# Performance work log

Hardware: AMD Instinct MI355X
Metric: run time of the kernel (lower is better)

## Reference

```python
import jax, jax.numpy as jnp
import numpy as np

B, T, C = 2, 2048, 1024
NH, NKV, HD = 16, 4, 64
VEC = 32  # ve_gate_channels


def _rope(x, cos, sin):
    d = x.shape[-1] // 2
    x1, x2 = x[..., :d], x[..., d:]
    return jnp.concatenate([x1 * cos + x2 * sin, -x1 * sin + x2 * cos], axis=-1)


def _rmsnorm(x):
    eps = jnp.finfo(x.dtype).eps
    return x * jax.lax.rsqrt(jnp.mean(x * x, axis=-1, keepdims=True) + eps)


def setup_inputs() -> dict:
    key = jax.random.key(0)
    ks = jax.random.split(key, 9)
    s = 0.02
    return {
        "x": jax.random.normal(ks[0], (B, T, C), jnp.float32),
        "ve": jax.random.normal(ks[1], (B, T, NKV * HD), jnp.float32),
        "cos": jax.random.normal(ks[2], (1, T, 1, HD // 2), jnp.float32),
        "sin": jax.random.normal(ks[3], (1, T, 1, HD // 2), jnp.float32),
        "Wq": jax.random.normal(ks[4], (C, NH * HD), jnp.float32) * s,
        "Wk": jax.random.normal(ks[5], (C, NKV * HD), jnp.float32) * s,
        "Wv": jax.random.normal(ks[6], (C, NKV * HD), jnp.float32) * s,
        "Wproj": jax.random.normal(ks[7], (C, C), jnp.float32) * s,
        "Wgate": jax.random.normal(ks[8], (VEC, NKV), jnp.float32) * s,
        "window_size": 1024,
    }


def reference(x, ve, cos, sin, Wq, Wk, Wv, Wproj, Wgate, window_size):
    Bx, Tx, Cx = x.shape
    q = (x @ Wq).reshape(Bx, Tx, NH, HD)
    k = (x @ Wk).reshape(Bx, Tx, NKV, HD)
    v = (x @ Wv).reshape(Bx, Tx, NKV, HD)

    # value-embedding gate (has_ve True for this layer)
    gate = 2.0 * jax.nn.sigmoid(x[..., :VEC] @ Wgate)  # [B,T,NKV]
    v = v + gate[..., None] * ve.reshape(Bx, Tx, NKV, HD)

    q, k = _rope(q, cos, sin), _rope(k, cos, sin)
    q, k = _rmsnorm(q), _rmsnorm(k)

    q = q.transpose(0, 2, 1, 3)  # [B,NH,T,HD]
    k = k.transpose(0, 2, 1, 3)  # [B,NKV,T,HD]
    v = v.transpose(0, 2, 1, 3)

    # GQA: each KV head serves NH//NKV consecutive q heads
    g = NH // NKV
    k = jnp.repeat(k, g, axis=1)
    v = jnp.repeat(v, g, axis=1)

    row = jnp.arange(Tx)[:, None]
    col = jnp.arange(Tx)[None, :]
    mask = (col <= row) & (col >= row - window_size)  # causal sliding window

    scores = jnp.einsum("bhqd,bhkd->bhqk", q, k) / np.sqrt(HD).astype(np.float32)
    scores = jnp.where(mask[None, None], scores, jnp.finfo(scores.dtype).min)
    attn = jax.nn.softmax(scores, axis=-1)
    y = jnp.einsum("bhqk,bhkd->bhqd", attn, v)

    y = y.transpose(0, 2, 1, 3).reshape(Bx, Tx, Cx)
    return y @ Wproj
```

## Files before the change

kernel.cpp:

```cpp
#include <hip/hip_runtime.h>

typedef __bf16 bf16x8 __attribute__((ext_vector_type(8)));
typedef __bf16 bf16x4 __attribute__((ext_vector_type(4)));
typedef float f32x4 __attribute__((ext_vector_type(4)));

__device__ inline float tof(float v) { return v; }
__device__ inline float tof(__bf16 v) { return (float)v; }

__device__ inline bf16x8 load8(const __bf16* p) { return *(const bf16x8*)p; }
__device__ inline bf16x8 load8(const float* p) {
    const float4 a = *(const float4*)p;
    const float4 b = *(const float4*)(p + 4);
    bf16x8 r;
    r[0] = (__bf16)a.x; r[1] = (__bf16)a.y; r[2] = (__bf16)a.z; r[3] = (__bf16)a.w;
    r[4] = (__bf16)b.x; r[5] = (__bf16)b.y; r[6] = (__bf16)b.z; r[7] = (__bf16)b.w;
    return r;
}

__device__ __forceinline__ float ldT(const void* p, size_t i, int isf32) {
    return isf32 ? ((const float*)p)[i] : tof(((const __bf16*)p)[i]);
}

__device__ __forceinline__ void cp16(__bf16* lds, const __bf16* g) {
    __builtin_amdgcn_global_load_lds((__attribute__((address_space(1))) void*)g,
                                     (__attribute__((address_space(3))) void*)lds,
                                     16, 0, 0);
}

__device__ __forceinline__ int sniff_block(const void* xraw) {
    const unsigned short* xs = (const unsigned short*)xraw;
    int tid = threadIdx.x;
    int bad = 0;
#pragma unroll
    for (int k = 0; k < 2; ++k) {
        float v = __uint_as_float(((unsigned int)xs[tid * 2 + k]) << 16);
        float a = fabsf(v);
        if (!(a <= 1e4f) || (a != 0.f && a < 1e-6f)) bad = 1;
    }
    return __syncthreads_count(bad) > 32;
}

template <typename T>
__device__ __forceinline__ void prep_body(
    const T* __restrict__ Wq, const T* __restrict__ Wk,
    const T* __restrict__ Wv, const T* __restrict__ Wp, const T* __restrict__ Wg,
    __bf16* __restrict__ WqT, __bf16* __restrict__ WkT,
    __bf16* __restrict__ WvT, __bf16* __restrict__ WpT,
    __bf16* __restrict__ wgb, __bf16* tile)
{
    const int b = blockIdx.x, tid = threadIdx.x;
    if (b < 640) {
        int idx = b;
        const T* src; __bf16* dst; int C;
        if (idx < 256)      { src = Wq; dst = WqT; C = 1024; }
        else if (idx < 320) { src = Wk; dst = WkT; C = 256;  idx -= 256; }
        else if (idx < 384) { src = Wv; dst = WvT; C = 256;  idx -= 320; }
        else                { src = Wp; dst = WpT; C = 1024; idx -= 384; }
        const int ctiles = C >> 6;
        const int r0 = (idx / ctiles) * 64, c0 = (idx % ctiles) * 64;
#pragma unroll
        for (int i = 0; i < 2; ++i) {
            int c = tid + i * 256, ir = c >> 3, ic = (c & 7) * 8;
            *(bf16x8*)(&tile[ir * 72 + ic]) = load8(src + (size_t)(r0 + ir) * C + c0 + ic);
        }
        __syncthreads();
#pragma unroll
        for (int i = 0; i < 2; ++i) {
            int c = tid + i * 256, orr = c >> 3, okc = (c & 7) * 8;
            bf16x8 v;
#pragma unroll
            for (int j = 0; j < 8; ++j) v[j] = tile[(okc + j) * 72 + orr];
            *(bf16x8*)(dst + (size_t)(c0 + orr) * 1024 + r0 + okc) = v;
        }
    } else if (tid < 128) {
        wgb[tid] = (__bf16)tof(Wg[tid]);
    }
}

__global__ __launch_bounds__(256) void prep_kernel(
    const void* x,
    const void* Wq, const void* Wk, const void* Wv, const void* Wp, const void* Wg,
    __bf16* WqT, __bf16* WkT, __bf16* WvT, __bf16* WpT, __bf16* wgb)
{
    __shared__ __bf16 tile[64 * 72];
    const int isf32 = sniff_block(x);
    if (isf32) {
        prep_body<float>((const float*)Wq, (const float*)Wk, (const float*)Wv,
                         (const float*)Wp, (const float*)Wg,
                         WqT, WkT, WvT, WpT, wgb, tile);
    } else {
        prep_body<__bf16>((const __bf16*)Wq, (const __bf16*)Wk, (const __bf16*)Wv,
                          (const __bf16*)Wp, (const __bf16*)Wg,
                          WqT, WkT, WvT, WpT, wgb, tile);
    }
}

__global__ __launch_bounds__(256) void qkv_kernel(
    const void* __restrict__ xraw, const void* __restrict__ veraw,
    const void* __restrict__ cosraw, const void* __restrict__ sinraw,
    const __bf16* __restrict__ WqT, const __bf16* __restrict__ WkT,
    const __bf16* __restrict__ WvT, const __bf16* __restrict__ wgb,
    __bf16* __restrict__ qo, __bf16* __restrict__ ko, __bf16* __restrict__ vTo)
{
    const int isf32 = sniff_block(xraw);
    const __bf16* xb = (const __bf16*)xraw;
    const float*  xf = (const float*)xraw;

    const int row0 = blockIdx.x * 128;
    const int cb = blockIdx.y;
    const __bf16* BT; int col0, h, mode;
    if (cb < 16)      { BT = WqT; col0 = cb * 64;        h = cb;      mode = 0; }
    else if (cb < 20) { BT = WkT; col0 = (cb - 16) * 64; h = cb - 16; mode = 1; }
    else              { BT = WvT; col0 = (cb - 20) * 64; h = cb - 20; mode = 2; }

    __shared__ __align__(16) __bf16 As[2][128 * 64];
    __shared__ __align__(16) __bf16 Bs[2][64 * 64];

    const int tid  = threadIdx.x;
    const int w    = tid >> 6;
    const int lane = tid & 63;
    const int quad = lane >> 4;
    const int l15  = lane & 15;
    const int wr   = w * 32;

    f32x4 acc[2][4];
#pragma unroll
    for (int mi = 0; mi < 2; ++mi)
#pragma unroll
        for (int nj = 0; nj < 4; ++nj) acc[mi][nj] = (f32x4){0.f, 0.f, 0.f, 0.f};

    bf16x8 wgB;
#pragma unroll
    for (int j = 0; j < 8; ++j) wgB[j] = (__bf16)0.f;
    if (mode == 2 && l15 < 4) {
#pragma unroll
        for (int j = 0; j < 8; ++j) wgB[j] = wgb[(quad * 8 + j) * 4 + l15];
    }
    f32x4 zacc[2];
    zacc[0] = (f32x4){0.f, 0.f, 0.f, 0.f};
    zacc[1] = (f32x4){0.f, 0.f, 0.f, 0.f};

    auto stageA_bf = [&](int buf, int kk) {
#pragma unroll
        for (int i = 0; i < 4; ++i) {
            int c = i * 256 + tid;
            cp16(&As[buf][c * 8], &xb[(size_t)(row0 + (c >> 3)) * 1024 + kk + ((c & 7) << 3)]);
        }
    };
    auto stageA_f32 = [&](int buf, int kk) {
#pragma unroll
        for (int i = 0; i < 4; ++i) {
            int c = i * 256 + tid;
            *(bf16x8*)(&As[buf][c * 8]) = load8(&xf[(size_t)(row0 + (c >> 3)) * 1024 + kk + ((c & 7) << 3)]);
        }
    };
    auto stageB = [&](int buf, int kk) {
#pragma unroll
        for (int i = 0; i < 2; ++i) {
            int c = i * 256 + tid;
            cp16(&Bs[buf][c * 8], &BT[(size_t)(col0 + (c >> 3)) * 1024 + kk + ((c & 7) << 3)]);
        }
    };

    if (isf32) stageA_f32(0, 0); else stageA_bf(0, 0);
    stageB(0, 0);
    __syncthreads();

    for (int kk = 0; kk < 1024; kk += 64) {
        const int cur = (kk >> 6) & 1;
        const bool more = (kk + 64 < 1024);
        if (more) {
            if (isf32) stageA_f32(cur ^ 1, kk + 64); else stageA_bf(cur ^ 1, kk + 64);
            stageB(cur ^ 1, kk + 64);
        }

        bf16x8 a[2][2], bfr[4][2];
#pragma unroll
        for (int mi = 0; mi < 2; ++mi)
#pragma unroll
            for (int kh = 0; kh < 2; ++kh)
                a[mi][kh] = *(const bf16x8*)(&As[cur][(wr + mi * 16 + l15) * 64 + kh * 32 + quad * 8]);
#pragma unroll
        for (int nj = 0; nj < 4; ++nj)
#pragma unroll
            for (int kh = 0; kh < 2; ++kh)
                bfr[nj][kh] = *(const bf16x8*)(&Bs[cur][(nj * 16 + l15) * 64 + kh * 32 + quad * 8]);

        if (mode == 2 && kk == 0) {
            zacc[0] = __builtin_amdgcn_mfma_f32_16x16x32_bf16(a[0][0], wgB, zacc[0], 0, 0, 0);
            zacc[1] = __builtin_amdgcn_mfma_f32_16x16x32_bf16(a[1][0], wgB, zacc[1], 0, 0, 0);
        }
#pragma unroll
        for (int kh = 0; kh < 2; ++kh)
#pragma unroll
            for (int mi = 0; mi < 2; ++mi)
#pragma unroll
                for (int nj = 0; nj < 4; ++nj)
                    acc[mi][nj] = __builtin_amdgcn_mfma_f32_16x16x32_bf16(a[mi][kh], bfr[nj][kh], acc[mi][nj], 0, 0, 0);
        __syncthreads();
    }

    if (mode < 2) {
        __bf16* dst = (mode == 0) ? qo : ko;
        const int nh = (mode == 0) ? 16 : 4;
        const float post = (mode == 0) ? 0.18033688f : 1.0f;
#pragma unroll
        for (int mi = 0; mi < 2; ++mi) {
#pragma unroll
            for (int r = 0; r < 4; ++r) {
                int row = row0 + wr + mi * 16 + quad * 4 + r;
                int b = row >> 11, t = row & 2047;
                float c0 = ldT(cosraw, t * 32 + l15, isf32);
                float c1 = ldT(cosraw, t * 32 + 16 + l15, isf32);
                float s0 = ldT(sinraw, t * 32 + l15, isf32);
                float s1 = ldT(sinraw, t * 32 + 16 + l15, isf32);
                float v0 =  c0 * acc[mi][0][r] + s0 * acc[mi][2][r];
                float v1 =  c1 * acc[mi][1][r] + s1 * acc[mi][3][r];
                float v2 = -s0 * acc[mi][0][r] + c0 * acc[mi][2][r];
                float v3 = -s1 * acc[mi][1][r] + c1 * acc[mi][3][r];
                float ss = v0 * v0 + v1 * v1 + v2 * v2 + v3 * v3;
                ss += __shfl_xor(ss, 1); ss += __shfl_xor(ss, 2);
                ss += __shfl_xor(ss, 4); ss += __shfl_xor(ss, 8);
                float sc = rsqrtf(ss * (1.f / 64.f) + 1.1920929e-7f) * post;
                size_t base = (((size_t)b * nh + h) * 2048 + t) * 64;
                dst[base + 0 * 16 + l15] = (__bf16)(v0 * sc);
                dst[base + 1 * 16 + l15] = (__bf16)(v1 * sc);
                dst[base + 2 * 16 + l15] = (__bf16)(v2 * sc);
                dst[base + 3 * 16 + l15] = (__bf16)(v3 * sc);
            }
        }
    } else {
#pragma unroll
        for (int mi = 0; mi < 2; ++mi) {
            int rowb = row0 + wr + mi * 16 + quad * 4;
            int b = rowb >> 11, t0 = rowb & 2047;
            float gg[4];
#pragma unroll
            for (int r = 0; r < 4; ++r) {
                float zv = __shfl(zacc[mi][r], quad * 16 + h);
                gg[r] = 2.f / (1.f + __expf(-zv));
            }
#pragma unroll
            for (int nj = 0; nj < 4; ++nj) {
                int d = nj * 16 + l15;
                bf16x4 pack;
#pragma unroll
                for (int r = 0; r < 4; ++r) {
                    int row = rowb + r;
                    float vev = ldT(veraw, (size_t)row * 256 + h * 64 + d, isf32);
                    pack[r] = (__bf16)(acc[mi][nj][r] + gg[r] * vev);
                }
                size_t a = (((size_t)b * 4 + h) * 64 + d) * 2048 + t0;
                *(bf16x4*)(&vTo[a]) = pack;
            }
        }
    }
}

__global__ __launch_bounds__(256) void attn_kernel(
    const __bf16* __restrict__ qg, const __bf16* __restrict__ kg,
    const __bf16* __restrict__ vTg, __bf16* __restrict__ yo,
    const int* __restrict__ winp)
{
    const int q0 = blockIdx.x * 128;
    const int hh = blockIdx.y, b = blockIdx.z;
    const int kvh = hh >> 2;
    const int W = winp[0];

    const int tid  = threadIdx.x;
    const int w    = tid >> 6;
    const int lane = tid & 63;
    const int quad = lane >> 4;
    const int l15  = lane & 15;

    __shared__ __align__(16) __bf16 Ks[2][64 * 64];
    __shared__ __align__(16) __bf16 Vt[2][64 * 64];
    __shared__ __align__(16) __bf16 Ps[4][32 * 72];

    bf16x8 qf[2][2];
#pragma unroll
    for (int i = 0; i < 2; ++i) {
        size_t qb = (((size_t)b * 16 + hh) * 2048 + q0 + w * 32 + i * 16 + l15) * 64;
        qf[i][0] = *(const bf16x8*)(&qg[qb + quad * 8]);
        qf[i][1] = *(const bf16x8*)(&qg[qb + 32 + quad * 8]);
    }

    f32x4 oacc[2][4];
    float lsum[2][4];
#pragma unroll
    for (int i = 0; i < 2; ++i)
#pragma unroll
        for (int n = 0; n < 4; ++n) {
            oacc[i][n] = (f32x4){0.f, 0.f, 0.f, 0.f};
            lsum[i][n] = 0.f;
        }

    const int lo = q0 - W;
    const int kt_lo = lo > 0 ? (lo >> 6) : 0;
    const int kt_hi = (q0 + 127) >> 6;
    const size_t kvbase = ((size_t)b * 4 + kvh) * 2048 * 64;

    auto stage = [&](int buf, int k0) {
#pragma unroll
        for (int i = 0; i < 2; ++i) {
            int c = i * 256 + tid;
            int rr = c >> 3;
            int jj = (c & 7) ^ (rr & 7);
            cp16(&Ks[buf][c * 8], &kg[kvbase + (size_t)(k0 + rr) * 64 + jj * 8]);
            cp16(&Vt[buf][c * 8], &vTg[kvbase + (size_t)rr * 2048 + k0 + jj * 8]);
        }
    };

    stage(0, kt_lo * 64);
    __syncthreads();

    int cur = 0;
    for (int kt = kt_lo; kt <= kt_hi; ++kt) {
        const int k0 = kt * 64;
        const bool need_mask = (k0 + 63 > q0) || (q0 + 127 - k0 > W);
        if (kt < kt_hi) stage(cur ^ 1, k0 + 64);

        f32x4 sacc[2][4];
#pragma unroll
        for (int i = 0; i < 2; ++i)
#pragma unroll
            for (int n = 0; n < 4; ++n) sacc[i][n] = (f32x4){0.f, 0.f, 0.f, 0.f};
        const __bf16* Kc = &Ks[cur][0];
#pragma unroll
        for (int n = 0; n < 4; ++n) {
            int m = n * 16 + l15;
            bf16x8 b0 = *(const bf16x8*)(&Kc[m * 64 + (quad ^ (m & 7)) * 8]);
            bf16x8 b1 = *(const bf16x8*)(&Kc[m * 64 + ((4 + quad) ^ (m & 7)) * 8]);
#pragma unroll
            for (int i = 0; i < 2; ++i) {
                sacc[i][n] = __builtin_amdgcn_mfma_f32_16x16x32_bf16(qf[i][0], b0, sacc[i][n], 0, 0, 0);
                sacc[i][n] = __builtin_amdgcn_mfma_f32_16x16x32_bf16(qf[i][1], b1, sacc[i][n], 0, 0, 0);
            }
        }

#pragma unroll
        for (int i = 0; i < 2; ++i) {
#pragma unroll
            for (int r = 0; r < 4; ++r) {
                const int row_g = q0 + w * 32 + i * 16 + quad * 4 + r;
#pragma unroll
                for (int n = 0; n < 4; ++n) {
                    float p = exp2f(sacc[i][n][r]);
                    if (need_mask) {
                        int col_g = k0 + n * 16 + l15;
                        bool ok = (col_g <= row_g) && (row_g - col_g <= W);
                        p = ok ? p : 0.f;
                    }
                    lsum[i][r] += p;
                    Ps[w][(i * 16 + quad * 4 + r) * 72 + n * 16 + l15] = (__bf16)p;
                }
            }
        }
        asm volatile("s_waitcnt lgkmcnt(0)" ::: "memory");

        const __bf16* Vc = &Vt[cur][0];
#pragma unroll
        for (int ks = 0; ks < 2; ++ks) {
            bf16x8 pfr0 = *(const bf16x8*)(&Ps[w][l15 * 72 + ks * 32 + quad * 8]);
            bf16x8 pfr1 = *(const bf16x8*)(&Ps[w][(16 + l15) * 72 + ks * 32 + quad * 8]);
#pragma unroll
            for (int n = 0; n < 4; ++n) {
                int m = n * 16 + l15;
                bf16x8 bv = *(const bf16x8*)(&Vc[m * 64 + ((ks * 4 + quad) ^ (m & 7)) * 8]);
                oacc[0][n] = __builtin_amdgcn_mfma_f32_16x16x32_bf16(pfr0, bv, oacc[0][n], 0, 0, 0);
                oacc[1][n] = __builtin_amdgcn_mfma_f32_16x16x32_bf16(pfr1, bv, oacc[1][n], 0, 0, 0);
            }
        }

        __syncthreads();
        cur ^= 1;
    }

#pragma unroll
    for (int i = 0; i < 2; ++i) {
#pragma unroll
        for (int r = 0; r < 4; ++r) {
            float l = lsum[i][r];
            l += __shfl_xor(l, 1); l += __shfl_xor(l, 2);
            l += __shfl_xor(l, 4); l += __shfl_xor(l, 8);
            float inv = 1.f / l;
            int t = q0 + w * 32 + i * 16 + quad * 4 + r;
            size_t base = ((size_t)(b * 2048 + t)) * 1024 + hh * 64;
#pragma unroll
            for (int n = 0; n < 4; ++n)
                yo[base + n * 16 + l15] = (__bf16)(oacc[i][n][r] * inv);
        }
    }
}

__global__ __launch_bounds__(256) void proj_kernel(
    const __bf16* __restrict__ y, const __bf16* __restrict__ WpT,
    void* __restrict__ outp, const void* __restrict__ xraw)
{
    const int isf32 = sniff_block(xraw);
    const int row0 = blockIdx.x * 128;
    const int col0 = blockIdx.y * 64;
    __shared__ __align__(16) __bf16 As[2][128 * 64];
    __shared__ __align__(16) __bf16 Bs[2][64 * 64];

    const int tid  = threadIdx.x;
    const int w    = tid >> 6;
    const int lane = tid & 63;
    const int quad = lane >> 4;
    const int l15  = lane & 15;
    const int wr   = w * 32;

    f32x4 acc[2][4];
#pragma unroll
    for (int mi = 0; mi < 2; ++mi)
#pragma unroll
        for (int nj = 0; nj < 4; ++nj) acc[mi][nj] = (f32x4){0.f, 0.f, 0.f, 0.f};

    auto stage = [&](int buf, int kk) {
#pragma unroll
        for (int i = 0; i < 4; ++i) {
            int c = i * 256 + tid;
            cp16(&As[buf][c * 8], &y[(size_t)(row0 + (c >> 3)) * 1024 + kk + ((c & 7) << 3)]);
        }
#pragma unroll
        for (int i = 0; i < 2; ++i) {
            int c = i * 256 + tid;
            cp16(&Bs[buf][c * 8], &WpT[(size_t)(col0 + (c >> 3)) * 1024 + kk + ((c & 7) << 3)]);
        }
    };

    stage(0, 0);
    __syncthreads();

    for (int kk = 0; kk < 1024; kk += 64) {
        const int cur = (kk >> 6) & 1;
        if (kk + 64 < 1024) stage(cur ^ 1, kk + 64);

        bf16x8 a[2][2], bfr[4][2];
#pragma unroll
        for (int mi = 0; mi < 2; ++mi)
#pragma unroll
            for (int kh = 0; kh < 2; ++kh)
                a[mi][kh] = *(const bf16x8*)(&As[cur][(wr + mi * 16 + l15) * 64 + kh * 32 + quad * 8]);
#pragma unroll
        for (int nj = 0; nj < 4; ++nj)
#pragma unroll
            for (int kh = 0; kh < 2; ++kh)
                bfr[nj][kh] = *(const bf16x8*)(&Bs[cur][(nj * 16 + l15) * 64 + kh * 32 + quad * 8]);
#pragma unroll
        for (int kh = 0; kh < 2; ++kh)
#pragma unroll
            for (int mi = 0; mi < 2; ++mi)
#pragma unroll
                for (int nj = 0; nj < 4; ++nj)
                    acc[mi][nj] = __builtin_amdgcn_mfma_f32_16x16x32_bf16(a[mi][kh], bfr[nj][kh], acc[mi][nj], 0, 0, 0);
        __syncthreads();
    }

#pragma unroll
    for (int mi = 0; mi < 2; ++mi)
#pragma unroll
        for (int r = 0; r < 4; ++r) {
            int row = row0 + wr + mi * 16 + quad * 4 + r;
            if (isf32) {
                float* out = (float*)outp;
#pragma unroll
                for (int nj = 0; nj < 4; ++nj)
                    out[(size_t)row * 1024 + col0 + nj * 16 + l15] = acc[mi][nj][r];
            } else {
                __bf16* out = (__bf16*)outp;
#pragma unroll
                for (int nj = 0; nj < 4; ++nj)
                    out[(size_t)row * 1024 + col0 + nj * 16 + l15] = (__bf16)acc[mi][nj][r];
            }
        }
}

extern "C" void kernel_launch(void* const* d_in, const int* in_sizes, int n_in,
                              void* d_out, int out_size, void* d_ws, size_t ws_size,
                              hipStream_t stream) {
    const int* win = (const int*)d_in[9];

    char* p = (char*)d_ws;
    __bf16* q_ws = (__bf16*)p;                 p += (size_t)4194304 * 2;
    __bf16* k_ws = (__bf16*)p;                 p += (size_t)1048576 * 2;
    __bf16* vT_ws= (__bf16*)p;                 p += (size_t)1048576 * 2;
    __bf16* y_ws = (__bf16*)p;                 p += (size_t)4194304 * 2;
    __bf16* WqT  = (__bf16*)p;                 p += (size_t)1048576 * 2;
    __bf16* WkT  = (__bf16*)p;                 p += (size_t)262144 * 2;
    __bf16* WvT  = (__bf16*)p;                 p += (size_t)262144 * 2;
    __bf16* WpT  = (__bf16*)p;                 p += (size_t)1048576 * 2;
    __bf16* wgb  = (__bf16*)p;                 p += 256;

    prep_kernel<<<641, 256, 0, stream>>>(
        d_in[0], d_in[4], d_in[5], d_in[6], d_in[7], d_in[8],
        WqT, WkT, WvT, WpT, wgb);

    qkv_kernel<<<dim3(32, 24), 256, 0, stream>>>(
        d_in[0], d_in[1], d_in[2], d_in[3],
        WqT, WkT, WvT, wgb, q_ws, k_ws, vT_ws);

    attn_kernel<<<dim3(16, 16, 2), 256, 0, stream>>>(q_ws, k_ws, vT_ws, y_ws, win);

    proj_kernel<<<dim3(32, 16), 256, 0, stream>>>(y_ws, WpT, d_out, d_in[0]);
}
```

Baseline: 203.2 us.

## Pre-convert x to bf16 in prep kernel and balance attention block order

The prep kernel now also converts the fp32 input x to a bf16 workspace copy. The QKV GEMM can then always stage A tiles with async global-to-LDS loads, instead of every column block reloading and converting fp32 x through registers. The attention kernel also reverses the query-block order for the second batch, which mixes long and short sliding-window workloads across the grid. This costs an extra 8 MB write and read of x in bf16 and a larger prep launch.

```diff
diff --git a/kernel.cpp b/kernel.cpp
--- a/kernel.cpp
+++ b/kernel.cpp
@@ -42,15 +42,20 @@
 
 template <typename T>
 __device__ __forceinline__ void prep_body(
+    const T* __restrict__ x,
     const T* __restrict__ Wq, const T* __restrict__ Wk,
     const T* __restrict__ Wv, const T* __restrict__ Wp, const T* __restrict__ Wg,
+    __bf16* __restrict__ xb,
     __bf16* __restrict__ WqT, __bf16* __restrict__ WkT,
     __bf16* __restrict__ WvT, __bf16* __restrict__ WpT,
     __bf16* __restrict__ wgb, __bf16* tile)
 {
     const int b = blockIdx.x, tid = threadIdx.x;
-    if (b < 640) {
-        int idx = b;
+    if (b < 2048) {
+        int g = b * 256 + tid;
+        *(bf16x8*)(xb + (size_t)g * 8) = load8(x + (size_t)g * 8);
+    } else if (b < 2688) {
+        int idx = b - 2048;
         const T* src; __bf16* dst; int C;
         if (idx < 256)      { src = Wq; dst = WqT; C = 1024; }
         else if (idx < 320) { src = Wk; dst = WkT; C = 256;  idx -= 256; }
@@ -80,22 +85,24 @@
 __global__ __launch_bounds__(256) void prep_kernel(
     const void* x,
     const void* Wq, const void* Wk, const void* Wv, const void* Wp, const void* Wg,
+    __bf16* xb,
     __bf16* WqT, __bf16* WkT, __bf16* WvT, __bf16* WpT, __bf16* wgb)
 {
     __shared__ __bf16 tile[64 * 72];
     const int isf32 = sniff_block(x);
     if (isf32) {
-        prep_body<float>((const float*)Wq, (const float*)Wk, (const float*)Wv,
-                         (const float*)Wp, (const float*)Wg,
-                         WqT, WkT, WvT, WpT, wgb, tile);
+        prep_body<float>((const float*)x, (const float*)Wq, (const float*)Wk,
+                         (const float*)Wv, (const float*)Wp, (const float*)Wg,
+                         xb, WqT, WkT, WvT, WpT, wgb, tile);
     } else {
-        prep_body<__bf16>((const __bf16*)Wq, (const __bf16*)Wk, (const __bf16*)Wv,
-                          (const __bf16*)Wp, (const __bf16*)Wg,
-                          WqT, WkT, WvT, WpT, wgb, tile);
+        prep_body<__bf16>((const __bf16*)x, (const __bf16*)Wq, (const __bf16*)Wk,
+                          (const __bf16*)Wv, (const __bf16*)Wp, (const __bf16*)Wg,
+                          xb, WqT, WkT, WvT, WpT, wgb, tile);
     }
 }
 
 __global__ __launch_bounds__(256) void qkv_kernel(
+    const __bf16* __restrict__ xb,
     const void* __restrict__ xraw, const void* __restrict__ veraw,
     const void* __restrict__ cosraw, const void* __restrict__ sinraw,
     const __bf16* __restrict__ WqT, const __bf16* __restrict__ WkT,
@@ -103,8 +110,6 @@
     __bf16* __restrict__ qo, __bf16* __restrict__ ko, __bf16* __restrict__ vTo)
 {
     const int isf32 = sniff_block(xraw);
-    const __bf16* xb = (const __bf16*)xraw;
-    const float*  xf = (const float*)xraw;
 
     const int row0 = blockIdx.x * 128;
     const int cb = blockIdx.y;
@@ -140,21 +145,12 @@
     zacc[0] = (f32x4){0.f, 0.f, 0.f, 0.f};
     zacc[1] = (f32x4){0.f, 0.f, 0.f, 0.f};
 
-    auto stageA_bf = [&](int buf, int kk) {
+    auto stage = [&](int buf, int kk) {
 #pragma unroll
         for (int i = 0; i < 4; ++i) {
             int c = i * 256 + tid;
             cp16(&As[buf][c * 8], &xb[(size_t)(row0 + (c >> 3)) * 1024 + kk + ((c & 7) << 3)]);
         }
-    };
-    auto stageA_f32 = [&](int buf, int kk) {
-#pragma unroll
-        for (int i = 0; i < 4; ++i) {
-            int c = i * 256 + tid;
-            *(bf16x8*)(&As[buf][c * 8]) = load8(&xf[(size_t)(row0 + (c >> 3)) * 1024 + kk + ((c & 7) << 3)]);
-        }
-    };
-    auto stageB = [&](int buf, int kk) {
 #pragma unroll
         for (int i = 0; i < 2; ++i) {
             int c = i * 256 + tid;
@@ -162,17 +158,12 @@
         }
     };
 
-    if (isf32) stageA_f32(0, 0); else stageA_bf(0, 0);
-    stageB(0, 0);
+    stage(0, 0);
     __syncthreads();
 
     for (int kk = 0; kk < 1024; kk += 64) {
         const int cur = (kk >> 6) & 1;
-        const bool more = (kk + 64 < 1024);
-        if (more) {
-            if (isf32) stageA_f32(cur ^ 1, kk + 64); else stageA_bf(cur ^ 1, kk + 64);
-            stageB(cur ^ 1, kk + 64);
-        }
+        if (kk + 64 < 1024) stage(cur ^ 1, kk + 64);
 
         bf16x8 a[2][2], bfr[4][2];
 #pragma unroll
@@ -262,8 +253,10 @@
     const __bf16* __restrict__ vTg, __bf16* __restrict__ yo,
     const int* __restrict__ winp)
 {
-    const int q0 = blockIdx.x * 128;
-    const int hh = blockIdx.y, b = blockIdx.z;
+    const int b = blockIdx.z;
+    const int qb = b ? (15 - blockIdx.x) : blockIdx.x;
+    const int q0 = qb * 128;
+    const int hh = blockIdx.y;
     const int kvh = hh >> 2;
     const int W = winp[0];
 
@@ -280,9 +273,9 @@
     bf16x8 qf[2][2];
 #pragma unroll
     for (int i = 0; i < 2; ++i) {
-        size_t qb = (((size_t)b * 16 + hh) * 2048 + q0 + w * 32 + i * 16 + l15) * 64;
-        qf[i][0] = *(const bf16x8*)(&qg[qb + quad * 8]);
-        qf[i][1] = *(const bf16x8*)(&qg[qb + 32 + quad * 8]);
+        size_t qb_ = (((size_t)b * 16 + hh) * 2048 + q0 + w * 32 + i * 16 + l15) * 64;
+        qf[i][0] = *(const bf16x8*)(&qg[qb_ + quad * 8]);
+        qf[i][1] = *(const bf16x8*)(&qg[qb_ + 32 + quad * 8]);
     }
 
     f32x4 oacc[2][4];
@@ -486,18 +479,19 @@
     __bf16* k_ws = (__bf16*)p;                 p += (size_t)1048576 * 2;
     __bf16* vT_ws= (__bf16*)p;                 p += (size_t)1048576 * 2;
     __bf16* y_ws = (__bf16*)p;                 p += (size_t)4194304 * 2;
+    __bf16* xb   = (__bf16*)p;                 p += (size_t)4194304 * 2;
     __bf16* WqT  = (__bf16*)p;                 p += (size_t)1048576 * 2;
     __bf16* WkT  = (__bf16*)p;                 p += (size_t)262144 * 2;
     __bf16* WvT  = (__bf16*)p;                 p += (size_t)262144 * 2;
     __bf16* WpT  = (__bf16*)p;                 p += (size_t)1048576 * 2;
     __bf16* wgb  = (__bf16*)p;                 p += 256;
 
-    prep_kernel<<<641, 256, 0, stream>>>(
+    prep_kernel<<<2689, 256, 0, stream>>>(
         d_in[0], d_in[4], d_in[5], d_in[6], d_in[7], d_in[8],
-        WqT, WkT, WvT, WpT, wgb);
+        xb, WqT, WkT, WvT, WpT, wgb);
 
     qkv_kernel<<<dim3(32, 24), 256, 0, stream>>>(
-        d_in[0], d_in[1], d_in[2], d_in[3],
+        xb, d_in[0], d_in[1], d_in[2], d_in[3],
         WqT, WkT, WvT, wgb, q_ws, k_ws, vT_ws);
 
     attn_kernel<<<dim3(16, 16, 2), 256, 0, stream>>>(q_ws, k_ws, vT_ws, y_ws, win);
```

Result: faster. 193.5 us (-4.8%).
